# Kernel tuning notes

Hardware: AMD Instinct MI355X
Metric: run time of the kernel (lower is better)

The kernel has to match this reference:

```python
import jax, jax.numpy as jnp
import numpy as np

N = 50000      # nodes
E = 800000     # edges (before self-loops)
F_IN = 256     # num_features (one-hot width / embedding rows)
D = 150        # embedding_dim
H = 2          # heads
C = 150        # hidden_channels per head
EPS = 1e-5


def gat_layer(h, src, dst, W, a_s, a_d, b):
    # h: [N, F], W: [F, H*C], a_s/a_d: [H, C], b: [H*C]
    hp = (h @ W).reshape(N, H, C)                      # projected per-head features
    al_s = (hp * a_s).sum(-1)                          # [N, H] source attention terms
    al_d = (hp * a_d).sum(-1)                          # [N, H] destination attention terms
    e = jax.nn.leaky_relu(al_s[src] + al_d[dst], 0.2)  # [Etot, H] edge logits
    m = jax.ops.segment_max(e, dst, num_segments=N)    # stable segment softmax over dst
    ex = jnp.exp(e - m[dst])
    denom = jax.ops.segment_sum(ex, dst, num_segments=N)
    alpha = ex / denom[dst]                            # [Etot, H]
    out = jax.ops.segment_sum(alpha[:, :, None] * hp[src], dst, num_segments=N)
    return out.reshape(N, H * C) + b                   # concat heads + bias


def setup_inputs() -> dict:
    key = jax.random.key(0)
    ks = jax.random.split(key, 16)
    g = lambda i, shape, s=0.05: jax.random.normal(ks[i], shape, dtype=jnp.float32) * s
    return {
        "x": jax.random.normal(ks[0], (N, F_IN), dtype=jnp.float32),
        "edge_index": jax.random.randint(ks[1], (2, E), 0, N),
        "edge_weight": jax.random.normal(ks[2], (E,), dtype=jnp.float32),
        "emb": g(3, (F_IN, D), 1.0),
        "W1": g(4, (D, H * C)),
        "a_src1": g(5, (H, C)),
        "a_dst1": g(6, (H, C)),
        "b1": jnp.zeros((H * C,), jnp.float32),
        "ln_g": jnp.ones((H * C,), jnp.float32),
        "ln_b": jnp.zeros((H * C,), jnp.float32),
        "W2": g(7, (H * C, H * C)),
        "a_src2": g(8, (H, C)),
        "a_dst2": g(9, (H, C)),
        "b2": jnp.zeros((H * C,), jnp.float32),
        "fc_w": g(10, (H * C, 1)),
        "fc_b": jnp.zeros((1,), jnp.float32),
    }


def reference(x, edge_index, edge_weight, emb, W1, a_src1, a_dst1, b1,
              ln_g, ln_b, W2, a_src2, a_dst2, b2, fc_w, fc_b):
    # edge_weight is accepted but unused: GATConv with edge_dim=None ignores edge_attr.
    idx = jnp.argmax(x, axis=1)
    h = emb[idx]                                       # [N, D]
    loops = jnp.arange(N)                              # GATConv add_self_loops=True
    src = jnp.concatenate([edge_index[0], loops])
    dst = jnp.concatenate([edge_index[1], loops])
    h = gat_layer(h, src, dst, W1, a_src1, a_dst1, b1)  # [N, H*C]
    mu = jnp.mean(h, axis=-1, keepdims=True)
    var = jnp.var(h, axis=-1, keepdims=True)
    h = (h - mu) * jax.lax.rsqrt(var + EPS) * ln_g + ln_b
    h = jax.nn.leaky_relu(h, 0.01)                      # dropout = identity (eval)
    h = jax.nn.leaky_relu(gat_layer(h, src, dst, W2, a_src2, a_dst2, b2), 0.01)
    return (h @ fc_w + fc_b).squeeze(-1)                # [N]
```

## Files before the change

### kernel.cpp

```cpp
#include <hip/hip_runtime.h>
#include <hip/hip_bf16.h>
#include <math.h>

#define NN 50000
#define EE 800000
#define FIN 256
#define DD 150
#define HC 300
#define CC 150
#define ET (EE + NN)
#define LN_EPS 1e-5f
#define NT 19

typedef __attribute__((ext_vector_type(8))) short short8;
typedef __attribute__((ext_vector_type(4))) float f32x4;
typedef unsigned short u16;
typedef unsigned int u32;

static __device__ __forceinline__ u16 f2bf(float f) {
  u32 u = __float_as_uint(f);
  u += 0x7FFFu + ((u >> 16) & 1u);
  return (u16)(u >> 16);
}
static __device__ __forceinline__ float bflo(u32 u) {
  return __uint_as_float(u << 16);
}
static __device__ __forceinline__ float bfhi(u32 u) {
  return __uint_as_float(u & 0xFFFF0000u);
}

__global__ __launch_bounds__(256) void k_argmax_embed(
    const float* __restrict__ x, const float* __restrict__ emb,
    u16* __restrict__ h0b) {
  int node = blockIdx.x * 4 + (threadIdx.x >> 6);
  int lane = threadIdx.x & 63;
  if (node >= NN) return;
  const float* row = x + (size_t)node * FIN;
  float best = -INFINITY;
  int bidx = FIN;
  #pragma unroll
  for (int r = 0; r < FIN / 64; ++r) {
    int j = lane + 64 * r;
    float v = row[j];
    if (v > best || (v == best && j < bidx)) { best = v; bidx = j; }
  }
  #pragma unroll
  for (int off = 32; off > 0; off >>= 1) {
    float ov = __shfl_xor(best, off, 64);
    int   oi = __shfl_xor(bidx, off, 64);
    if (ov > best || (ov == best && oi < bidx)) { best = ov; bidx = oi; }
  }
  const float2* e2 = (const float2*)(emb + (size_t)bidx * DD);
  u32* o = (u32*)(h0b + (size_t)node * DD);
  float2 v = e2[lane];
  o[lane] = (u32)f2bf(v.x) | ((u32)f2bf(v.y) << 16);
  if (lane < 11) {
    float2 w = e2[64 + lane];
    o[64 + lane] = (u32)f2bf(w.x) | ((u32)f2bf(w.y) << 16);
  }
}

__global__ __launch_bounds__(256) void k_count(
    const int* __restrict__ ei, int* __restrict__ counts) {
  int et = blockIdx.x * blockDim.x + threadIdx.x;
  if (et >= ET) return;
  int d = (et < EE) ? ei[EE + et] : (et - EE);
  atomicAdd(&counts[d], 1);
}

__global__ __launch_bounds__(1024) void k_scan(
    const int* __restrict__ counts, int* __restrict__ offsets) {
  __shared__ int buf[1024];
  const int CH = 49;
  int tid = threadIdx.x;
  int base = tid * CH;
  int lsum = 0;
  for (int c = 0; c < CH; ++c) {
    int i = base + c;
    if (i < NN) lsum += counts[i];
  }
  buf[tid] = lsum;
  __syncthreads();
  for (int off = 1; off < 1024; off <<= 1) {
    int t = (tid >= off) ? buf[tid - off] : 0;
    __syncthreads();
    buf[tid] += t;
    __syncthreads();
  }
  int incl = buf[tid];
  int run = incl - lsum;
  for (int c = 0; c < CH; ++c) {
    int i = base + c;
    if (i < NN) { offsets[i] = run; run += counts[i]; }
  }
  if (tid == 1023) offsets[NN] = incl;
}

__global__ __launch_bounds__(256) void k_scatter(
    const int* __restrict__ ei, const int* __restrict__ offsets,
    int* __restrict__ cursor, int* __restrict__ csr_src) {
  int et = blockIdx.x * blockDim.x + threadIdx.x;
  if (et >= ET) return;
  int s = (et < EE) ? ei[et] : (et - EE);
  int d = (et < EE) ? ei[EE + et] : (et - EE);
  int pos = offsets[d] + atomicAdd(&cursor[d], 1);
  csr_src[pos] = s;
}

__global__ __launch_bounds__(64) void k_pack_w(
    const float* __restrict__ W, u16* __restrict__ Wp, int K) {
  int ks = blockIdx.x / NT, ct = blockIdx.x % NT;
  int l = threadIdx.x;
  int col = ct * 16 + (l & 15);
  int kb = ks * 32 + ((l >> 4) << 3);
  u16 v[8];
  #pragma unroll
  for (int j = 0; j < 8; ++j) {
    int k = kb + j;
    float f = (k < K && col < HC) ? W[(size_t)k * HC + col] : 0.f;
    v[j] = f2bf(f);
  }
  *(ulonglong2*)(Wp + ((size_t)blockIdx.x * 64 + l) * 8) = *(ulonglong2*)v;
}

template <int K>
__global__ __launch_bounds__(256) void k_gemm_mfma(
    const u16* __restrict__ h, const u16* __restrict__ Wp,
    const float* __restrict__ a_s, const float* __restrict__ a_d,
    u16* __restrict__ hpb, float* __restrict__ al_s,
    float* __restrict__ al_d) {
  constexpr int KS = (K + 31) / 32;
  constexpr int RS = KS * 32 + 8;
  constexpr int KU = K / 2;
  constexpr int ZU = (KS * 32 - K) / 2;
  __shared__ u16 sh[64 * RS];
  int tid = threadIdx.x;
  int wave = tid >> 6, lane = tid & 63;
  int rows0 = blockIdx.x * 64;

  const u32* hu = (const u32*)h;
  for (int i = tid; i < 64 * KU; i += 256) {
    int r = i / KU, c = i - r * KU;
    int gr = rows0 + r; if (gr >= NN) gr = NN - 1;
    *(u32*)&sh[r * RS + 2 * c] = hu[(size_t)gr * KU + c];
  }
  for (int i = tid; i < 64 * ZU; i += 256) {
    int r = i / ZU, c = i - r * ZU;
    *(u32*)&sh[r * RS + K + 2 * c] = 0u;
  }
  __syncthreads();

  f32x4 acc[NT];
  #pragma unroll
  for (int ct = 0; ct < NT; ++ct) acc[ct] = f32x4{0.f, 0.f, 0.f, 0.f};

  const u16* abase = &sh[(wave * 16 + (lane & 15)) * RS + (lane >> 4) * 8];
  const short8* wb = (const short8*)Wp;

  short8 a = *(const short8*)abase;
  #pragma unroll 1
  for (int ks = 0; ks < KS; ++ks) {
    short8 an = (ks + 1 < KS) ? *(const short8*)(abase + (ks + 1) * 32) : a;
    #pragma unroll
    for (int ct = 0; ct < NT; ++ct) {
      short8 b = wb[(ks * NT + ct) * 64 + lane];
      acc[ct] = __builtin_amdgcn_mfma_f32_16x16x32_bf16(a, b, acc[ct], 0, 0, 0);
    }
    a = an;
  }

  int grow = rows0 + wave * 16 + ((lane >> 4) << 2);
  int cbase = lane & 15;

  float ps0[4] = {0, 0, 0, 0}, ps1[4] = {0, 0, 0, 0};
  float pd0[4] = {0, 0, 0, 0}, pd1[4] = {0, 0, 0, 0};
  #pragma unroll
  for (int ct = 0; ct < NT; ++ct) {
    int col = ct * 16 + cbase;
    bool valid = col < HC;
    bool head0 = col < CC;
    float as_v = valid ? a_s[col] : 0.f;
    float ad_v = valid ? a_d[col] : 0.f;
    #pragma unroll
    for (int j = 0; j < 4; ++j) {
      float v = acc[ct][j];
      int gr = grow + j;
      if (valid && gr < NN) hpb[(size_t)gr * HC + col] = f2bf(v);
      if (head0) { ps0[j] += v * as_v; pd0[j] += v * ad_v; }
      else       { ps1[j] += v * as_v; pd1[j] += v * ad_v; }
    }
  }
  #pragma unroll
  for (int o = 1; o < 16; o <<= 1) {
    #pragma unroll
    for (int j = 0; j < 4; ++j) {
      ps0[j] += __shfl_xor(ps0[j], o, 64);
      ps1[j] += __shfl_xor(ps1[j], o, 64);
      pd0[j] += __shfl_xor(pd0[j], o, 64);
      pd1[j] += __shfl_xor(pd1[j], o, 64);
    }
  }
  if ((lane & 15) == 0) {
    #pragma unroll
    for (int j = 0; j < 4; ++j) {
      int gr = grow + j;
      if (gr < NN) {
        ((float2*)al_s)[gr] = make_float2(ps0[j], ps1[j]);
        ((float2*)al_d)[gr] = make_float2(pd0[j], pd1[j]);
      }
    }
  }
}

__device__ __forceinline__ float lrelu(float v, float sl) {
  return v >= 0.f ? v : sl * v;
}

__device__ __forceinline__ void sm_combine(float& m, float& s, float om, float os) {
  if (om > m) {
    s = s * expf(m - om) + os;
    m = om;
  } else if (os > 0.f) {
    s += os * expf(om - m);
  }
}

__global__ __launch_bounds__(256) void k_stats_alpha(
    const float* __restrict__ al_s, const float* __restrict__ al_d,
    const int* __restrict__ offsets, const int* __restrict__ csr_src,
    float2* __restrict__ alpha2) {
  int node = blockIdx.x * 4 + (threadIdx.x >> 6);
  int lane = threadIdx.x & 63;
  if (node >= NN) return;
  int off = offsets[node];
  int deg = offsets[node + 1] - off;
  const float2* al2 = (const float2*)al_s;
  float2 aldv = ((const float2*)al_d)[node];
  float ald0 = aldv.x, ald1 = aldv.y;

  float m0 = -INFINITY, s0 = 0.f, m1 = -INFINITY, s1 = 0.f;
  for (int i = lane; i < deg; i += 64) {
    int sn = csr_src[off + i];
    float2 av = al2[sn];
    float e0 = lrelu(av.x + ald0, 0.2f);
    float e1 = lrelu(av.y + ald1, 0.2f);
    if (e0 > m0) { s0 = s0 * expf(m0 - e0) + 1.f; m0 = e0; } else s0 += expf(e0 - m0);
    if (e1 > m1) { s1 = s1 * expf(m1 - e1) + 1.f; m1 = e1; } else s1 += expf(e1 - m1);
  }
  #pragma unroll
  for (int o = 32; o > 0; o >>= 1) {
    float om0 = __shfl_xor(m0, o, 64), os0 = __shfl_xor(s0, o, 64);
    float om1 = __shfl_xor(m1, o, 64), os1 = __shfl_xor(s1, o, 64);
    sm_combine(m0, s0, om0, os0);
    sm_combine(m1, s1, om1, os1);
  }
  float inv0 = 1.f / s0, inv1 = 1.f / s1;

  for (int i = lane; i < deg; i += 64) {
    int sn = csr_src[off + i];
    float2 av = al2[sn];
    float e0 = lrelu(av.x + ald0, 0.2f);
    float e1 = lrelu(av.y + ald1, 0.2f);
    alpha2[off + i] = make_float2(expf(e0 - m0) * inv0, expf(e1 - m1) * inv1);
  }
}

__device__ __forceinline__ void agg_b(
    const u16* __restrict__ hpb, const int* __restrict__ csr_src,
    const float2* __restrict__ alpha2, int off, int deg, int lane,
    float4& o0, float4& o1) {
  o0 = make_float4(0.f, 0.f, 0.f, 0.f);
  o1 = make_float4(0.f, 0.f, 0.f, 0.f);
  int c0 = lane * 4;
  bool t0 = c0 + 0 < CC, t1 = c0 + 1 < CC, t2 = c0 + 2 < CC, t3 = c0 + 3 < CC;
  bool hi = lane < 11;

  int sn = csr_src[off];
  float2 al = alpha2[off];
  const uint2* rp = (const uint2*)(hpb + (size_t)sn * HC);
  uint2 u = rp[lane];
  uint2 ut = make_uint2(0u, 0u);
  if (hi) ut = rp[64 + lane];

  for (int i = 0; i < deg; ++i) {
    float2 nal = make_float2(0.f, 0.f);
    uint2 nu = make_uint2(0u, 0u), nut = make_uint2(0u, 0u);
    if (i + 1 < deg) {
      int nsn = csr_src[off + i + 1];
      nal = alpha2[off + i + 1];
      const uint2* nrp = (const uint2*)(hpb + (size_t)nsn * HC);
      nu = nrp[lane];
      if (hi) nut = nrp[64 + lane];
    }
    float a0 = al.x, a1 = al.y;
    o0.x += bflo(u.x) * (t0 ? a0 : a1);
    o0.y += bfhi(u.x) * (t1 ? a0 : a1);
    o0.z += bflo(u.y) * (t2 ? a0 : a1);
    o0.w += bfhi(u.y) * (t3 ? a0 : a1);
    o1.x += bflo(ut.x) * a1;
    o1.y += bfhi(ut.x) * a1;
    o1.z += bflo(ut.y) * a1;
    o1.w += bfhi(ut.y) * a1;
    u = nu; ut = nut; al = nal;
  }
}

__global__ __launch_bounds__(256) void k_agg_ln(
    const u16* __restrict__ hpb, const int* __restrict__ offsets,
    const int* __restrict__ csr_src, const float2* __restrict__ alpha2,
    const float* __restrict__ b1, const float* __restrict__ ln_g,
    const float* __restrict__ ln_b, u16* __restrict__ h1b) {
  int node = blockIdx.x * 4 + (threadIdx.x >> 6);
  int lane = threadIdx.x & 63;
  if (node >= NN) return;
  int off = offsets[node];
  int deg = offsets[node + 1] - off;

  float4 o0, o1;
  agg_b(hpb, csr_src, alpha2, off, deg, lane, o0, o1);

  const float4* b14 = (const float4*)b1;
  float4 bb = b14[lane];
  o0.x += bb.x; o0.y += bb.y; o0.z += bb.z; o0.w += bb.w;
  if (lane < 11) {
    float4 bc = b14[64 + lane];
    o1.x += bc.x; o1.y += bc.y; o1.z += bc.z; o1.w += bc.w;
  }
  float part = o0.x + o0.y + o0.z + o0.w;
  if (lane < 11) part += o1.x + o1.y + o1.z + o1.w;
  #pragma unroll
  for (int o = 32; o > 0; o >>= 1) part += __shfl_xor(part, o, 64);
  float mu = part * (1.f / HC);
  float vp = (o0.x - mu) * (o0.x - mu) + (o0.y - mu) * (o0.y - mu) +
             (o0.z - mu) * (o0.z - mu) + (o0.w - mu) * (o0.w - mu);
  if (lane < 11)
    vp += (o1.x - mu) * (o1.x - mu) + (o1.y - mu) * (o1.y - mu) +
          (o1.z - mu) * (o1.z - mu) + (o1.w - mu) * (o1.w - mu);
  #pragma unroll
  for (int o = 32; o > 0; o >>= 1) vp += __shfl_xor(vp, o, 64);
  float rstd = 1.f / sqrtf(vp * (1.f / HC) + LN_EPS);

  const float4* g4 = (const float4*)ln_g;
  const float4* lb4 = (const float4*)ln_b;
  u32* h1u = (u32*)(h1b + (size_t)node * HC);
  float4 g = g4[lane], lb = lb4[lane];
  float wx = lrelu((o0.x - mu) * rstd * g.x + lb.x, 0.01f);
  float wy = lrelu((o0.y - mu) * rstd * g.y + lb.y, 0.01f);
  float wz = lrelu((o0.z - mu) * rstd * g.z + lb.z, 0.01f);
  float ww = lrelu((o0.w - mu) * rstd * g.w + lb.w, 0.01f);
  h1u[2 * lane + 0] = (u32)f2bf(wx) | ((u32)f2bf(wy) << 16);
  h1u[2 * lane + 1] = (u32)f2bf(wz) | ((u32)f2bf(ww) << 16);
  if (lane < 11) {
    float4 g1 = g4[64 + lane], lb1 = lb4[64 + lane];
    float vx = lrelu((o1.x - mu) * rstd * g1.x + lb1.x, 0.01f);
    float vy = lrelu((o1.y - mu) * rstd * g1.y + lb1.y, 0.01f);
    float vz = lrelu((o1.z - mu) * rstd * g1.z + lb1.z, 0.01f);
    float vw = lrelu((o1.w - mu) * rstd * g1.w + lb1.w, 0.01f);
    h1u[2 * (64 + lane) + 0] = (u32)f2bf(vx) | ((u32)f2bf(vy) << 16);
    h1u[2 * (64 + lane) + 1] = (u32)f2bf(vz) | ((u32)f2bf(vw) << 16);
  }
}

__global__ __launch_bounds__(256) void k_agg_fc(
    const u16* __restrict__ hpb, const int* __restrict__ offsets,
    const int* __restrict__ csr_src, const float2* __restrict__ alpha2,
    const float* __restrict__ b2, const float* __restrict__ fc_w,
    const float* __restrict__ fc_b, float* __restrict__ outp) {
  int node = blockIdx.x * 4 + (threadIdx.x >> 6);
  int lane = threadIdx.x & 63;
  if (node >= NN) return;
  int off = offsets[node];
  int deg = offsets[node + 1] - off;

  float4 o0, o1;
  agg_b(hpb, csr_src, alpha2, off, deg, lane, o0, o1);

  const float4* b24 = (const float4*)b2;
  const float4* f4 = (const float4*)fc_w;
  float4 bb = b24[lane], fw = f4[lane];
  float acc = lrelu(o0.x + bb.x, 0.01f) * fw.x +
              lrelu(o0.y + bb.y, 0.01f) * fw.y +
              lrelu(o0.z + bb.z, 0.01f) * fw.z +
              lrelu(o0.w + bb.w, 0.01f) * fw.w;
  if (lane < 11) {
    float4 bc = b24[64 + lane], fc = f4[64 + lane];
    acc += lrelu(o1.x + bc.x, 0.01f) * fc.x +
           lrelu(o1.y + bc.y, 0.01f) * fc.y +
           lrelu(o1.z + bc.z, 0.01f) * fc.z +
           lrelu(o1.w + bc.w, 0.01f) * fc.w;
  }
  #pragma unroll
  for (int o = 32; o > 0; o >>= 1) acc += __shfl_xor(acc, o, 64);
  if (lane == 0) outp[node] = acc + fc_b[0];
}

static inline size_t align_up(size_t x, size_t a) { return (x + a - 1) & ~(a - 1); }

extern "C" void kernel_launch(void* const* d_in, const int* in_sizes, int n_in,
                              void* d_out, int out_size, void* d_ws, size_t ws_size,
                              hipStream_t stream) {
  const float* x    = (const float*)d_in[0];
  const int*   ei   = (const int*)d_in[1];
  const float* emb  = (const float*)d_in[3];
  const float* W1   = (const float*)d_in[4];
  const float* as1  = (const float*)d_in[5];
  const float* ad1  = (const float*)d_in[6];
  const float* b1   = (const float*)d_in[7];
  const float* ln_g = (const float*)d_in[8];
  const float* ln_b = (const float*)d_in[9];
  const float* W2   = (const float*)d_in[10];
  const float* as2  = (const float*)d_in[11];
  const float* ad2  = (const float*)d_in[12];
  const float* b2   = (const float*)d_in[13];
  const float* fc_w = (const float*)d_in[14];
  const float* fc_b = (const float*)d_in[15];
  float* outp = (float*)d_out;

  constexpr int KS1 = (DD + 31) / 32;
  constexpr int KS2 = (HC + 31) / 32;

  char* ws = (char*)d_ws;
  size_t o = 0;
  size_t o_hpb = o; o = align_up(o + (size_t)NN * HC * 2, 256);
  size_t o_h1b = o; o = align_up(o + (size_t)NN * HC * 2, 256);
  size_t o_als = o; o = align_up(o + (size_t)NN * 2 * 4, 256);
  size_t o_ald = o; o = align_up(o + (size_t)NN * 2 * 4, 256);
  size_t o_alp = o; o = align_up(o + (size_t)ET * 8, 256);
  size_t o_cnt = o; o = align_up(o + (size_t)NN * 4, 256);
  size_t o_cur = o; o = align_up(o + (size_t)NN * 4, 256);
  size_t o_off = o; o = align_up(o + (size_t)(NN + 1) * 4, 256);
  size_t o_csr = o; o = align_up(o + (size_t)ET * 4, 256);
  size_t o_wp1 = o; o = align_up(o + (size_t)KS1 * NT * 64 * 8 * 2, 256);
  size_t o_wp2 = o; o = align_up(o + (size_t)KS2 * NT * 64 * 8 * 2, 256);

  u16*   hpb     = (u16*)(ws + o_hpb);
  u16*   h1b     = (u16*)(ws + o_h1b);
  u16*   h0b     = (u16*)(ws + o_h1b);
  float* al_s    = (float*)(ws + o_als);
  float* al_d    = (float*)(ws + o_ald);
  float2* alpha2 = (float2*)(ws + o_alp);
  int*   counts  = (int*)(ws + o_cnt);
  int*   cursor  = (int*)(ws + o_cur);
  int*   offsets = (int*)(ws + o_off);
  int*   csr_src = (int*)(ws + o_csr);
  u16*   Wp1     = (u16*)(ws + o_wp1);
  u16*   Wp2     = (u16*)(ws + o_wp2);

  hipMemsetAsync(ws + o_cnt, 0, o_off - o_cnt, stream);

  const int nwave_blocks = (NN + 3) / 4;
  const int edge_blocks  = (ET + 255) / 256;
  const int gemm_blocks  = (NN + 63) / 64;

  k_argmax_embed<<<nwave_blocks, 256, 0, stream>>>(x, emb, h0b);
  k_count<<<edge_blocks, 256, 0, stream>>>(ei, counts);
  k_scan<<<1, 1024, 0, stream>>>(counts, offsets);
  k_scatter<<<edge_blocks, 256, 0, stream>>>(ei, offsets, cursor, csr_src);
  k_pack_w<<<KS1 * NT, 64, 0, stream>>>(W1, Wp1, DD);
  k_pack_w<<<KS2 * NT, 64, 0, stream>>>(W2, Wp2, HC);

  k_gemm_mfma<DD><<<gemm_blocks, 256, 0, stream>>>(h0b, Wp1, as1, ad1,
                                                   hpb, al_s, al_d);
  k_stats_alpha<<<nwave_blocks, 256, 0, stream>>>(al_s, al_d, offsets,
                                                  csr_src, alpha2);
  k_agg_ln<<<nwave_blocks, 256, 0, stream>>>(hpb, offsets, csr_src, alpha2,
                                             b1, ln_g, ln_b, h1b);

  k_gemm_mfma<HC><<<gemm_blocks, 256, 0, stream>>>(h1b, Wp2, as2, ad2,
                                                   hpb, al_s, al_d);
  k_stats_alpha<<<nwave_blocks, 256, 0, stream>>>(al_s, al_d, offsets,
                                                  csr_src, alpha2);
  k_agg_fc<<<nwave_blocks, 256, 0, stream>>>(hpb, offsets, csr_src, alpha2,
                                             b2, fc_w, fc_b, outp);
}
```

Baseline: 695.5 us.

## Replace single-block CSR offset scan with three-phase multi-block scan

The exclusive prefix sum over per-node edge counts used to run in one 1024-thread block, with each thread reading 49 strided counts serially. It becomes three kernels: per-block reductions over 49 blocks, a single-wave shuffle scan of the block totals, and a per-block scan that adds the block prefix and writes offsets, including offsets[NN]. This spreads the work across many CUs and makes the count reads coalesced. In exchange it adds two kernel launches and a small partials buffer in the workspace.

```diff
diff --git a/kernel.cpp b/kernel.cpp
--- a/kernel.cpp
+++ b/kernel.cpp
@@ -11,6 +11,7 @@
 #define ET (EE + NN)
 #define LN_EPS 1e-5f
 #define NT 19
+#define NB 49
 
 typedef __attribute__((ext_vector_type(8))) short short8;
 typedef __attribute__((ext_vector_type(4))) float f32x4;
@@ -68,32 +69,51 @@
   atomicAdd(&counts[d], 1);
 }
 
-__global__ __launch_bounds__(1024) void k_scan(
-    const int* __restrict__ counts, int* __restrict__ offsets) {
+__global__ __launch_bounds__(1024) void k_part(
+    const int* __restrict__ counts, int* __restrict__ partial) {
+  __shared__ int red[1024];
+  int tid = threadIdx.x;
+  int i = blockIdx.x * 1024 + tid;
+  red[tid] = (i < NN) ? counts[i] : 0;
+  __syncthreads();
+  for (int off = 512; off > 0; off >>= 1) {
+    if (tid < off) red[tid] += red[tid + off];
+    __syncthreads();
+  }
+  if (tid == 0) partial[blockIdx.x] = red[0];
+}
+
+__global__ __launch_bounds__(64) void k_scan_part(
+    const int* __restrict__ partial, int* __restrict__ pexc) {
+  int t = threadIdx.x;
+  int v = (t < NB) ? partial[t] : 0;
+  int incl = v;
+  #pragma unroll
+  for (int off = 1; off < 64; off <<= 1) {
+    int n = __shfl_up(incl, off, 64);
+    if (t >= off) incl += n;
+  }
+  if (t < NB) pexc[t] = incl - v;
+}
+
+__global__ __launch_bounds__(1024) void k_scan_apply(
+    const int* __restrict__ counts, const int* __restrict__ pexc,
+    int* __restrict__ offsets) {
   __shared__ int buf[1024];
-  const int CH = 49;
-  int tid = threadIdx.x;
-  int base = tid * CH;
-  int lsum = 0;
-  for (int c = 0; c < CH; ++c) {
-    int i = base + c;
-    if (i < NN) lsum += counts[i];
-  }
-  buf[tid] = lsum;
+  int b = blockIdx.x, tid = threadIdx.x;
+  int i = b * 1024 + tid;
+  int v = (i < NN) ? counts[i] : 0;
+  buf[tid] = v;
   __syncthreads();
+  int incl = v;
   for (int off = 1; off < 1024; off <<= 1) {
     int t = (tid >= off) ? buf[tid - off] : 0;
     __syncthreads();
-    buf[tid] += t;
+    incl += t;
+    buf[tid] = incl;
     __syncthreads();
   }
-  int incl = buf[tid];
-  int run = incl - lsum;
-  for (int c = 0; c < CH; ++c) {
-    int i = base + c;
-    if (i < NN) { offsets[i] = run; run += counts[i]; }
-  }
-  if (tid == 1023) offsets[NN] = incl;
+  if (i <= NN) offsets[i] = pexc[b] + incl - v;
 }
 
 __global__ __launch_bounds__(256) void k_scatter(
@@ -432,6 +452,8 @@
   size_t o_csr = o; o = align_up(o + (size_t)ET * 4, 256);
   size_t o_wp1 = o; o = align_up(o + (size_t)KS1 * NT * 64 * 8 * 2, 256);
   size_t o_wp2 = o; o = align_up(o + (size_t)KS2 * NT * 64 * 8 * 2, 256);
+  size_t o_par = o; o = align_up(o + (size_t)NB * 4, 256);
+  size_t o_pex = o; o = align_up(o + (size_t)(NB + 1) * 4, 256);
 
   u16*   hpb     = (u16*)(ws + o_hpb);
   u16*   h1b     = (u16*)(ws + o_h1b);
@@ -445,6 +467,8 @@
   int*   csr_src = (int*)(ws + o_csr);
   u16*   Wp1     = (u16*)(ws + o_wp1);
   u16*   Wp2     = (u16*)(ws + o_wp2);
+  int*   partial = (int*)(ws + o_par);
+  int*   pexc    = (int*)(ws + o_pex);
 
   hipMemsetAsync(ws + o_cnt, 0, o_off - o_cnt, stream);
 
@@ -454,7 +478,9 @@
 
   k_argmax_embed<<<nwave_blocks, 256, 0, stream>>>(x, emb, h0b);
   k_count<<<edge_blocks, 256, 0, stream>>>(ei, counts);
-  k_scan<<<1, 1024, 0, stream>>>(counts, offsets);
+  k_part<<<NB, 1024, 0, stream>>>(counts, partial);
+  k_scan_part<<<1, 64, 0, stream>>>(partial, pexc);
+  k_scan_apply<<<NB, 1024, 0, stream>>>(counts, pexc, offsets);
   k_scatter<<<edge_blocks, 256, 0, stream>>>(ei, offsets, cursor, csr_src);
   k_pack_w<<<KS1 * NT, 64, 0, stream>>>(W1, Wp1, DD);
   k_pack_w<<<KS2 * NT, 64, 0, stream>>>(W2, Wp2, HC);
```

Result: faster. 614.0 us (-11.7%).
